# Kernel optimization log

Hardware: AMD Instinct MI355X
Metric: run time of the kernel (lower is better)

Reference implementation:

```python
import jax, jax.numpy as jnp
import numpy as np

PRUNING_RATE = 0.1
ROPE_THETA = 10000.0
EPS = 1e-5


def _rms_norm(x, w):
    v = jnp.mean(jnp.square(x.astype(jnp.float32)), axis=-1, keepdims=True)
    return (x * jax.lax.rsqrt(v + EPS)).astype(x.dtype) * w


def _rotate_half(x):
    x1, x2 = jnp.split(x, 2, axis=-1)
    return jnp.concatenate([-x2, x1], axis=-1)


def setup_inputs() -> dict:
    key = jax.random.key(0)
    ks = jax.random.split(key, 11)
    B, Q, D, H, Dh, P, F = 2, 16, 2048, 16, 128, 8192, 5632
    K = P + Q
    s = D ** -0.5
    inp = {
        "hidden_states": jax.random.normal(ks[0], (B, Q, D), jnp.float32),
        "past_k": jax.random.normal(ks[1], (B, H, P, Dh), jnp.float32),
        "past_v": jax.random.normal(ks[2], (B, H, P, Dh), jnp.float32),
        "wq": jax.random.normal(ks[3], (D, D), jnp.float32) * s,
        "wk": jax.random.normal(ks[4], (D, D), jnp.float32) * s,
        "wv": jax.random.normal(ks[5], (D, D), jnp.float32) * s,
        "wo": jax.random.normal(ks[6], (D, D), jnp.float32) * s,
        "w_gate": jax.random.normal(ks[7], (D, F), jnp.float32) * s,
        "w_up": jax.random.normal(ks[8], (D, F), jnp.float32) * s,
        "w_down": jax.random.normal(ks[9], (F, D), jnp.float32) * (F ** -0.5),
        "norm1_w": jnp.ones((D,), jnp.float32),
        "norm2_w": jnp.ones((D,), jnp.float32),
    }
    # causal mask over [past + new] keys: query i (global pos P+i) sees keys <= P+i
    q_pos = P + jnp.arange(Q)
    k_pos = jnp.arange(K)
    mask = jnp.where(k_pos[None, :] <= q_pos[:, None], 0.0, -1e9).astype(jnp.float32)
    inp["attn_mask"] = jnp.broadcast_to(mask[None, None], (B, 1, Q, K))
    return inp


def reference(hidden_states, past_k, past_v, attn_mask, wq, wk, wv, wo,
              w_gate, w_up, w_down, norm1_w, norm2_w):
    B, Q, D = hidden_states.shape
    _, H, P, Dh = past_k.shape
    K = P + Q

    residual = hidden_states
    x = _rms_norm(hidden_states, norm1_w)
    q = (x @ wq).reshape(B, Q, H, Dh).transpose(0, 2, 1, 3)  # [B,H,Q,Dh]
    k = (x @ wk).reshape(B, Q, H, Dh).transpose(0, 2, 1, 3)
    v = (x @ wv).reshape(B, Q, H, Dh).transpose(0, 2, 1, 3)

    # RoPE at cache positions P..P+Q-1 (past keys already rotated)
    inv_freq = 1.0 / (ROPE_THETA ** (jnp.arange(0, Dh, 2, dtype=jnp.float32) / Dh))
    pos = (P + jnp.arange(Q)).astype(jnp.float32)
    emb = jnp.concatenate([pos[:, None] * inv_freq[None, :]] * 2, axis=-1)  # [Q,Dh]
    cos, sin = jnp.cos(emb), jnp.sin(emb)
    q = q * cos + _rotate_half(q) * sin
    k = k * cos + _rotate_half(k) * sin

    k_full = jnp.concatenate([past_k, k], axis=2)  # [B,H,K,Dh]
    v_full = jnp.concatenate([past_v, v], axis=2)

    scores = jnp.einsum("bhqd,bhkd->bhqk", q, k_full) / jnp.sqrt(jnp.float32(Dh))
    scores = scores + attn_mask
    attn = jax.nn.softmax(scores, axis=-1)  # eager weights (output_attentions=True)
    out = jnp.einsum("bhqk,bhkd->bhqd", attn, v_full)
    out = out.transpose(0, 2, 1, 3).reshape(B, Q, D) @ wo
    h = residual + out

    y = _rms_norm(h, norm2_w)
    new_hidden = h + (jax.nn.silu(y @ w_gate) * (y @ w_up)) @ w_down

    # importance-based KV eviction: mean attn to last query over batch*heads
    imp = jnp.sum(attn[:, :, Q - 1, :], axis=(0, 1)) / (B * H)  # [K]
    imp = imp.at[K - 1].set(jnp.inf)  # never evict the last token's key
    n_prune = int(PRUNING_RATE * K)
    _, prune_idxs = jax.lax.top_k(-imp, n_prune)  # smallest-importance keys
    return new_hidden, attn, prune_idxs
```

## Files before the change

### kernel.cpp

```cpp
#include <hip/hip_runtime.h>
#include <math.h>

#define BB 2
#define QQ 16
#define DD 2048
#define HH 16
#define DHH 128
#define PP 8192
#define FF 5632
#define KK 8208
#define BH 32
#define RR 32
#define NPRUNE 820

#define OFF_X      0u
#define OFF_QR     65536u
#define OFF_KN     131072u
#define OFF_VN     196608u
#define OFF_ROWM   262144u
#define OFF_ROWZ   262656u
#define OFF_OATTN  263168u
#define OFF_H      328704u
#define OFF_Y      394240u
#define OFF_ACT    459776u
#define OFF_UNION  640064u
#define OFF_F64    (OFF_UNION + 4456448u)
#define D_X64      0u
#define D_K64      65536u
#define D_Q64      131072u
#define D_M64      135168u
#define D_Z64      135200u
#define D_SC       135232u
#define D_KEYS     397888u
#define OFF_RANK   (OFF_F64 + 812192u)

__global__ __launch_bounds__(256) void rmsnorm_kernel(
    const float* __restrict__ in, const float* __restrict__ w,
    float* __restrict__ out)
{
    int r = blockIdx.x;
    const float* x = in + (size_t)r * DD;
    float ss = 0.f;
    for (int c = threadIdx.x; c < DD; c += 256) { float v = x[c]; ss = fmaf(v, v, ss); }
    __shared__ float red[256];
    red[threadIdx.x] = ss;
    __syncthreads();
    for (int off = 128; off > 0; off >>= 1) {
        if (threadIdx.x < off) red[threadIdx.x] += red[threadIdx.x + off];
        __syncthreads();
    }
    float mean = red[0] / (float)DD;
    float scale = 1.0f / sqrtf(mean + 1e-5f);
    for (int c = threadIdx.x; c < DD; c += 256)
        out[(size_t)r * DD + c] = x[c] * scale * w[c];
}

__global__ __launch_bounds__(64) void rms32mix_kernel(
    const float* __restrict__ in, const float* __restrict__ w,
    double* __restrict__ out)
{
    int r = blockIdx.x;
    const float* x = in + (size_t)r * DD;
    __shared__ float bs[16];
    __shared__ float sscale;
    int tid = threadIdx.x;
    if (tid < 16) {
        const float* a = x + tid * 128;
        float rr[8];
#pragma unroll
        for (int j = 0; j < 8; ++j) { float v = a[j]; rr[j] = __fmul_rn(v, v); }
        for (int i = 8; i < 128; i += 8) {
#pragma unroll
            for (int j = 0; j < 8; ++j) {
                float v = a[i + j];
                rr[j] = __fadd_rn(rr[j], __fmul_rn(v, v));
            }
        }
        float t01 = __fadd_rn(rr[0], rr[1]);
        float t23 = __fadd_rn(rr[2], rr[3]);
        float t45 = __fadd_rn(rr[4], rr[5]);
        float t67 = __fadd_rn(rr[6], rr[7]);
        bs[tid] = __fadd_rn(__fadd_rn(t01, t23), __fadd_rn(t45, t67));
    }
    __syncthreads();
    if (tid == 0) {
        float c[8], d[4], e[2];
#pragma unroll
        for (int i = 0; i < 8; ++i) c[i] = __fadd_rn(bs[2 * i], bs[2 * i + 1]);
#pragma unroll
        for (int i = 0; i < 4; ++i) d[i] = __fadd_rn(c[2 * i], c[2 * i + 1]);
        e[0] = __fadd_rn(d[0], d[1]);
        e[1] = __fadd_rn(d[2], d[3]);
        float s = __fadd_rn(e[0], e[1]);
        float v = __fdiv_rn(s, 2048.0f);
        float ve = __fadd_rn(v, 1e-5f);
        float sq = __fsqrt_rn(ve);
        sscale = __fdiv_rn(1.0f, sq);
    }
    __syncthreads();
    double scd = (double)sscale;
    for (int c = tid; c < DD; c += 64)
        out[(size_t)r * DD + c] = ((double)x[c] * scd) * (double)w[c];
}

__global__ __launch_bounds__(256) void proj64_part_kernel(
    const double* __restrict__ x64, const float* __restrict__ wk,
    const float* __restrict__ wq, double* __restrict__ part)
{
    int cc = blockIdx.x, kc = blockIdx.y;
    int tid = threadIdx.x;
    int col = cc * 256 + tid;
    int d0 = kc * 64;
    __shared__ double xs[34 * 64];
    for (int i = tid; i < 34 * 64; i += 256) {
        int r = i >> 6, d = i & 63;
        int srcrow = (r < 32) ? r : ((r == 32) ? 15 : 31);
        xs[i] = x64[(size_t)srcrow * DD + d0 + d];
    }
    __syncthreads();
    double acc[34];
#pragma unroll
    for (int r = 0; r < 34; ++r) acc[r] = 0.0;
    const float* wkp = wk + (size_t)d0 * DD + col;
    const float* wqp = wq + (size_t)d0 * DD + col;
    for (int d = 0; d < 64; d += 4) {
        double wkb[4], wqb[4];
#pragma unroll
        for (int u = 0; u < 4; ++u) {
            wkb[u] = (double)wkp[(size_t)(d + u) * DD];
            wqb[u] = (double)wqp[(size_t)(d + u) * DD];
        }
#pragma unroll
        for (int u = 0; u < 4; ++u) {
#pragma unroll
            for (int r = 0; r < 32; ++r) acc[r] = fma(xs[r * 64 + d + u], wkb[u], acc[r]);
            acc[32] = fma(xs[32 * 64 + d + u], wqb[u], acc[32]);
            acc[33] = fma(xs[33 * 64 + d + u], wqb[u], acc[33]);
        }
    }
#pragma unroll
    for (int r = 0; r < 34; ++r)
        part[((size_t)kc * 34 + r) * DD + col] = acc[r];
}

__global__ __launch_bounds__(256) void proj64_reduce_kernel(
    const double* __restrict__ part, double* __restrict__ k64,
    double* __restrict__ q64)
{
    int e = blockIdx.x * 256 + threadIdx.x;
    if (e >= 34 * DD) return;
    int r = e >> 11, col = e & 2047;
    double s = 0.0;
#pragma unroll 8
    for (int kc = 0; kc < 32; ++kc) s += part[((size_t)kc * 34 + r) * DD + col];
    if (r < 32) k64[(size_t)r * DD + col] = s;
    else        q64[(size_t)(r - 32) * DD + col] = s;
}

__global__ __launch_bounds__(256) void rope64_kernel(
    double* __restrict__ k64, double* __restrict__ q64)
{
    int r = blockIdx.x;
    double* row;
    int pos;
    if (r < 32) { row = k64 + (size_t)r * DD; pos = PP + (r & 15); }
    else        { row = q64 + (size_t)(r - 32) * DD; pos = PP + 15; }
#pragma unroll 4
    for (int i = 0; i < 4; ++i) {
        int p = threadIdx.x + 256 * i;
        int h = p >> 6, j = p & 63;
        float pf = (float)pow(10000.0, (double)j / 64.0);
        float invf = __fdiv_rn(1.0f, pf);
        float ang = __fmul_rn((float)pos, invf);
        float cs = (float)cos((double)ang);
        float sn = (float)sin((double)ang);
        int c1 = h * DHH + j, c2 = c1 + 64;
        double v1 = row[c1], v2 = row[c2];
        row[c1] = v1 * (double)cs - v2 * (double)sn;
        row[c2] = v2 * (double)cs + v1 * (double)sn;
    }
}

template<int DCHUNK>
__global__ __launch_bounds__(256) void gemm32c2(
    const float* __restrict__ A, const float* __restrict__ w0,
    const float* __restrict__ w1, const float* __restrict__ w2,
    float* __restrict__ part, int Kdim, int N, size_t zstride)
{
    int cc = blockIdx.x, kc = blockIdx.y, z = blockIdx.z;
    int tid = threadIdx.x;
    int col0 = cc * 512 + tid;
    int d0 = kc * DCHUNK;
    const float* W = (z == 0) ? w0 : (z == 1) ? w1 : w2;
    __shared__ __align__(16) float xs[32 * DCHUNK];
    for (int i = tid; i < 32 * DCHUNK; i += 256) {
        int r = i / DCHUNK, d = i - r * DCHUNK;
        xs[i] = A[(size_t)r * Kdim + d0 + d];
    }
    __syncthreads();
    float acc0[32], acc1[32];
#pragma unroll
    for (int r = 0; r < 32; ++r) { acc0[r] = 0.f; acc1[r] = 0.f; }
// ... 9 lines not shown
        for (int r = 0; r < 32; ++r) {
            const float4 x0 = *(const float4*)(xs + r * DCHUNK + d);
            const float4 x1 = *(const float4*)(xs + r * DCHUNK + d + 4);
            float a = acc0[r], b = acc1[r];
            a = fmaf(x0.x, wb0[0], a);  b = fmaf(x0.x, wb1[0], b);
            a = fmaf(x0.y, wb0[1], a);  b = fmaf(x0.y, wb1[1], b);
            a = fmaf(x0.z, wb0[2], a);  b = fmaf(x0.z, wb1[2], b);
            a = fmaf(x0.w, wb0[3], a);  b = fmaf(x0.w, wb1[3], b);
            a = fmaf(x1.x, wb0[4], a);  b = fmaf(x1.x, wb1[4], b);
            a = fmaf(x1.y, wb0[5], a);  b = fmaf(x1.y, wb1[5], b);
            a = fmaf(x1.z, wb0[6], a);  b = fmaf(x1.z, wb1[6], b);
            a = fmaf(x1.w, wb0[7], a);  b = fmaf(x1.w, wb1[7], b);
            acc0[r] = a; acc1[r] = b;
        }
    }
    float* dst = part + (size_t)z * zstride;
#pragma unroll
    for (int r = 0; r < 32; ++r) {
        dst[((size_t)(kc * 32 + r)) * N + col0] = acc0[r];
        dst[((size_t)(kc * 32 + r)) * N + col0 + 256] = acc1[r];
    }
}

__global__ __launch_bounds__(256) void reduce_qkv_rope(
    const float* __restrict__ part, float* __restrict__ qr,
    float* __restrict__ kn, float* __restrict__ vn)
{
    int r = blockIdx.x;
    int b = r >> 4, qi = r & 15;
    int tid = threadIdx.x;
    int c = blockIdx.y * 256 + tid;
    int h = c >> 7, dh = c & 127, j = dh & 63;

    float invf = (float)exp(-((double)j / 64.0) * log(10000.0));
    float ang = (float)(PP + qi) * invf;
    float sn, cs;
    sincosf(ang, &sn, &cs);

    __shared__ float buf[256];
    size_t dsti = (((size_t)(b * HH + h)) * QQ + qi) * DHH + dh;
    for (int mat = 0; mat < 3; ++mat) {
        const float* pm = part + (size_t)mat * 64 * 65536 + (size_t)r * DD + c;
        float sa = 0.f, sb = 0.f;
#pragma unroll 8
        for (int kc = 0; kc < 32; ++kc) {
            sa += pm[(size_t)kc * 32 * DD];
            sb += pm[(size_t)(kc + 32) * 32 * DD];
        }
        float s = sa + sb;
        buf[tid] = s;
        __syncthreads();
        float val;
        if (mat == 2) {
            val = s;
        } else {
            float other = (dh < 64) ? -buf[tid + 64] : buf[tid - 64];
            val = s * cs + other * sn;
        }
        float* dst = (mat == 0) ? qr : (mat == 1) ? kn : vn;
        dst[dsti] = val;
        __syncthreads();
    }
}

__global__ __launch_bounds__(256) void scores_kernel(
    const float* __restrict__ qr, const float* __restrict__ past_k,
    const float* __restrict__ kn, float* __restrict__ attn,
    const double* __restrict__ q64, const double* __restrict__ k64,
    double* __restrict__ sc64)
{
    int bh = blockIdx.x, ch = blockIdx.y;
    int b = bh >> 4, h = bh & 15;
    int tid = threadIdx.x;
    __shared__ __align__(16) float qs[QQ * DHH];
    __shared__ double q64s[DHH];
    for (int i = tid; i < QQ * DHH; i += 256) qs[i] = qr[(size_t)bh * (QQ * DHH) + i];
    if (tid < DHH) q64s[tid] = q64[(size_t)b * DD + h * DHH + tid];
    __syncthreads();

    if (ch < 16) {
        int kbase = ch * 512;
        const float* kr0 = past_k + ((size_t)bh * PP + kbase + tid) * DHH;
        float acc[2][QQ];
#pragma unroll
// ... 60 lines not shown
#pragma unroll
            for (int q = 0; q < QQ; ++q) {
                float4 qv = *(const float4*)(qs + q * DHH + j * 4);
                acc[q] = fmaf(kv.x, qv.x, acc[q]);
                acc[q] = fmaf(kv.y, qv.y, acc[q]);
                acc[q] = fmaf(kv.z, qv.z, acc[q]);
                acc[q] = fmaf(kv.w, qv.w, acc[q]);
            }
        }
        int key = PP + tid;
#pragma unroll
        for (int q = 0; q < QQ; ++q) {
            float sv = acc[q] / 11.313708498984761f;
            if (key > PP + q) sv += -1e9f;
            attn[((size_t)(bh * QQ + q)) * KK + key] = sv;
        }
        double a64 = 0.0;
        const double* kd = k64 + (size_t)(b * QQ + tid) * DD + h * DHH;
        for (int j = 0; j < DHH; ++j) a64 = fma(kd[j], q64s[j], a64);
        sc64[(size_t)bh * KK + key] = a64 / (double)sqrtf(128.0f);
    }
}

__global__ __launch_bounds__(256) void rowstats_kernel(
    const float* __restrict__ attn, float* __restrict__ rowm, float* __restrict__ rowz)
{
    int row = blockIdx.x;
    const float* s = attn + (size_t)row * KK;
    float m = -INFINITY, z = 0.f;
    for (int k = threadIdx.x; k < KK; k += 256) {
        float v = s[k];
        float nm = fmaxf(m, v);
        z = z * expf(m - nm) + expf(v - nm);
        m = nm;
    }
    __shared__ float sm[256], sz[256];
    sm[threadIdx.x] = m; sz[threadIdx.x] = z;
    __syncthreads();
    for (int off = 128; off > 0; off >>= 1) {
        if (threadIdx.x < off) {
            float m1 = sm[threadIdx.x], z1 = sz[threadIdx.x];
            float m2 = sm[threadIdx.x + off], z2 = sz[threadIdx.x + off];
            float nm = fmaxf(m1, m2);
            sm[threadIdx.x] = nm;
            sz[threadIdx.x] = z1 * expf(m1 - nm) + z2 * expf(m2 - nm);
        }
        __syncthreads();
    }
    if (threadIdx.x == 0) { rowm[row] = sm[0]; rowz[row] = sz[0]; }
}

__global__ __launch_bounds__(256) void rowstats64_kernel(
    const double* __restrict__ sc, double* __restrict__ m64, double* __restrict__ z64)
{
    int row = blockIdx.x;
    const double* s = sc + (size_t)row * KK;
    double m = -INFINITY, z = 0.0;
    for (int k = threadIdx.x; k < KK; k += 256) {
        double v = s[k];
        double nm = fmax(m, v);
        z = z * exp(m - nm) + exp(v - nm);
        m = nm;
    }
    __shared__ double sm[256], sz[256];
    sm[threadIdx.x] = m; sz[threadIdx.x] = z;
    __syncthreads();
    for (int off = 128; off > 0; off >>= 1) {
        if (threadIdx.x < off) {
            double m1 = sm[threadIdx.x], z1 = sz[threadIdx.x];
            double m2 = sm[threadIdx.x + off], z2 = sz[threadIdx.x + off];
            double nm = fmax(m1, m2);
            sm[threadIdx.x] = nm;
            sz[threadIdx.x] = z1 * exp(m1 - nm) + z2 * exp(m2 - nm);
        }
        __syncthreads();
    }
    if (threadIdx.x == 0) { m64[row] = sm[0]; z64[row] = sz[0]; }
}

__global__ __launch_bounds__(256) void impkeys_kernel(
    const double* __restrict__ sc, const double* __restrict__ m64,
    const double* __restrict__ z64, unsigned long long* __restrict__ keys,
    int* __restrict__ rank)
{
    int k = blockIdx.x * 256 + threadIdx.x;
    if (k >= KK) return;
    rank[k] = 0;
    double t = 0.0;
    for (int bh = 0; bh < BH; ++bh)
        t += exp(sc[(size_t)bh * KK + k] - m64[bh]) / z64[bh];
    double imp = t / 32.0;
    if (k == KK - 1) imp = INFINITY;
    unsigned long long bits = (unsigned long long)__double_as_longlong(imp);
    keys[k] = (bits & ~0x3FFFull) | (unsigned long long)k;
}

__global__ __launch_bounds__(256) void rankpart_kernel(
    const unsigned long long* __restrict__ keys, int* __restrict__ rank)
{
    __shared__ unsigned long long chnk[1026];
    int gid = blockIdx.x * 256 + threadIdx.x;
    int base = blockIdx.y * 1026;
    for (int i = threadIdx.x; i < 1026; i += 256) chnk[i] = keys[base + i];
    __syncthreads();
    if (gid >= KK) return;
    unsigned long long mykey = keys[gid];
    int cnt = 0;
#pragma unroll 6
    for (int i = 0; i < 1026; ++i) cnt += (chnk[i] < mykey) ? 1 : 0;
    atomicAdd(&rank[gid], cnt);
}

__global__ __launch_bounds__(256) void rankwrite_kernel(
    const unsigned long long* __restrict__ keys, const int* __restrict__ rank,
    float* __restrict__ outp)
{
    int gid = blockIdx.x * 256 + threadIdx.x;
    if (gid >= KK) return;
    int r = rank[gid];
    if (r < NPRUNE)
        outp[r] = (float)(unsigned)(keys[gid] & 0x3FFFu);
}

__global__ __launch_bounds__(256) void pv_kernel(
    float* __restrict__ attn, const float* __restrict__ past_v,
    const float* __restrict__ vn, const float* __restrict__ rowm,
    const float* __restrict__ rowz, float* __restrict__ part)
{
    int bh = blockIdx.x, ch = blockIdx.y;
    int tid = threadIdx.x;
    __shared__ __align__(16) float p[QQ * 256];
    int nk = (ch < 32) ? 256 : 16;
    int kbase = ch * 256;
    if (tid < nk) {
        float sv[QQ];
#pragma unroll
        for (int q = 0; q < QQ; ++q)
            sv[q] = attn[((size_t)(bh * QQ + q)) * KK + kbase + tid];
#pragma unroll
        for (int q = 0; q < QQ; ++q) {
            int row = bh * QQ + q;
            float pv = expf(sv[q] - rowm[row]) / rowz[row];
            attn[((size_t)row) * KK + kbase + tid] = pv;
            p[q * 256 + tid] = pv;
        }
    }
    __syncthreads();

    int dq = tid & 31, q0 = tid >> 5;
    int d4 = dq * 4;
    float4 a0 = make_float4(0, 0, 0, 0), a1 = make_float4(0, 0, 0, 0);
    if (ch < 32) {
        const float* vbase = past_v + ((size_t)bh * PP + kbase) * DHH;
        for (int kk = 0; kk < 256; kk += 8) {
            float4 vb[8];
#pragma unroll
            for (int u = 0; u < 8; ++u)
                vb[u] = *(const float4*)(vbase + (size_t)(kk + u) * DHH + d4);
#pragma unroll
            for (int u = 0; u < 8; ++u) {
                float p0 = p[q0 * 256 + kk + u];
                float p1 = p[(q0 + 8) * 256 + kk + u];
                a0.x = fmaf(vb[u].x, p0, a0.x); a0.y = fmaf(vb[u].y, p0, a0.y);
                a0.z = fmaf(vb[u].z, p0, a0.z); a0.w = fmaf(vb[u].w, p0, a0.w);
                a1.x = fmaf(vb[u].x, p1, a1.x); a1.y = fmaf(vb[u].y, p1, a1.y);
                a1.z = fmaf(vb[u].z, p1, a1.z); a1.w = fmaf(vb[u].w, p1, a1.w);
            }
        }
    } else {
        const float* vbase = vn + (size_t)bh * QQ * DHH;
        for (int kk = 0; kk < 16; ++kk) {
            float4 v4 = *(const float4*)(vbase + (size_t)kk * DHH + d4);
            float p0 = p[q0 * 256 + kk];
            float p1 = p[(q0 + 8) * 256 + kk];
            a0.x = fmaf(v4.x, p0, a0.x); a0.y = fmaf(v4.y, p0, a0.y);
            a0.z = fmaf(v4.z, p0, a0.z); a0.w = fmaf(v4.w, p0, a0.w);
            a1.x = fmaf(v4.x, p1, a1.x); a1.y = fmaf(v4.y, p1, a1.y);
            a1.z = fmaf(v4.z, p1, a1.z); a1.w = fmaf(v4.w, p1, a1.w);
        }
    }
    size_t pb = ((size_t)ch * BH + bh) * (QQ * DHH);
    *(float4*)(part + pb + q0 * DHH + d4) = a0;
    *(float4*)(part + pb + (q0 + 8) * DHH + d4) = a1;
}

__global__ __launch_bounds__(256) void pv_reduce_kernel(
    const float* __restrict__ part, float* __restrict__ oattn)
{
    int e = blockIdx.x * 256 + threadIdx.x;
    float sa = 0.f, sb = 0.f;
#pragma unroll 8
    for (int ch = 0; ch < 16; ++ch) sa += part[(size_t)ch * 65536 + e];
#pragma unroll 8
    for (int ch = 16; ch < 33; ++ch) sb += part[(size_t)ch * 65536 + e];
    float s = sa + sb;
    int bh = e >> 11, rem = e & 2047, q = rem >> 7, d = rem & 127;
    int b = bh >> 4, h = bh & 15;
    oattn[((size_t)(b * QQ + q)) * DD + h * DHH + d] = s;
}

__global__ __launch_bounds__(256) void reduce_wo_kernel(
    const float* __restrict__ part, const float* __restrict__ resid,
    float* __restrict__ hbuf)
{
    int e = blockIdx.x * 256 + threadIdx.x;
    float sa = 0.f, sb = 0.f;
#pragma unroll 8
    for (int kc = 0; kc < 32; ++kc) {
        sa += part[(size_t)kc * 65536 + e];
        sb += part[(size_t)(kc + 32) * 65536 + e];
    }
    hbuf[e] = resid[e] + (sa + sb);
}

__global__ __launch_bounds__(256) void reduce_gateup_silu_kernel(
    const float* __restrict__ part, float* __restrict__ act)
{
    int e = blockIdx.x * 256 + threadIdx.x;
    float ga = 0.f, gb = 0.f, ua = 0.f, ub = 0.f;
#pragma unroll 8
    for (int kc = 0; kc < 16; ++kc) {
// ... 22 lines not shown
}

extern "C" void kernel_launch(void* const* d_in, const int* in_sizes, int n_in,
                              void* d_out, int out_size, void* d_ws, size_t ws_size,
                              hipStream_t stream)
{
    const float* hidden = (const float*)d_in[0];
    const float* past_k = (const float*)d_in[1];
    const float* past_v = (const float*)d_in[2];
    const float* wq     = (const float*)d_in[3];
    const float* wk     = (const float*)d_in[4];
    const float* wv     = (const float*)d_in[5];
    const float* wo     = (const float*)d_in[6];
    const float* wgate  = (const float*)d_in[7];
    const float* wup    = (const float*)d_in[8];
    const float* wdown  = (const float*)d_in[9];
    const float* n1w    = (const float*)d_in[10];
    const float* n2w    = (const float*)d_in[11];

    float* out_hidden = (float*)d_out;
    float* attn = out_hidden + (size_t)RR * DD;
    float* out_prune = attn + (size_t)BH * QQ * KK;
    float* ws = (float*)d_ws;
    double* f64 = (double*)(ws + OFF_F64);
    double* x64 = f64 + D_X64;
    double* k64 = f64 + D_K64;
    double* q64 = f64 + D_Q64;
    double* m64 = f64 + D_M64;
    double* z64 = f64 + D_Z64;
    double* sc64 = f64 + D_SC;
    unsigned long long* keys = (unsigned long long*)(f64 + D_KEYS);
    int* rank = (int*)(ws + OFF_RANK);
    double* part64 = (double*)(ws + OFF_UNION);

    rmsnorm_kernel<<<dim3(RR), dim3(256), 0, stream>>>(hidden, n1w, ws + OFF_X);

    gemm32c2<32><<<dim3(4, 64, 3), dim3(256), 0, stream>>>(
        ws + OFF_X, wq, wk, wv, ws + OFF_UNION, DD, DD, (size_t)64 * 65536);

    reduce_qkv_rope<<<dim3(RR, 8), dim3(256), 0, stream>>>(
        ws + OFF_UNION, ws + OFF_QR, ws + OFF_KN, ws + OFF_VN);

    rms32mix_kernel<<<dim3(RR), dim3(64), 0, stream>>>(hidden, n1w, x64);
    proj64_part_kernel<<<dim3(8, 32), dim3(256), 0, stream>>>(x64, wk, wq, part64);
    proj64_reduce_kernel<<<dim3(272), dim3(256), 0, stream>>>(part64, k64, q64);
    rope64_kernel<<<dim3(34), dim3(256), 0, stream>>>(k64, q64);

    scores_kernel<<<dim3(BH, 17), dim3(256), 0, stream>>>(
        ws + OFF_QR, past_k, ws + OFF_KN, attn, q64, k64, sc64);

    rowstats_kernel<<<dim3(BH * QQ), dim3(256), 0, stream>>>(
        attn, ws + OFF_ROWM, ws + OFF_ROWZ);
    rowstats64_kernel<<<dim3(BH), dim3(256), 0, stream>>>(sc64, m64, z64);
    impkeys_kernel<<<dim3(33), dim3(256), 0, stream>>>(sc64, m64, z64, keys, rank);
    rankpart_kernel<<<dim3(33, 8), dim3(256), 0, stream>>>(keys, rank);
    rankwrite_kernel<<<dim3(33), dim3(256), 0, stream>>>(keys, rank, out_prune);

    pv_kernel<<<dim3(BH, 33), dim3(256), 0, stream>>>(
        attn, past_v, ws + OFF_VN, ws + OFF_ROWM, ws + OFF_ROWZ, ws + OFF_UNION);

    pv_reduce_kernel<<<dim3(256), dim3(256), 0, stream>>>(ws + OFF_UNION, ws + OFF_OATTN);

    gemm32c2<32><<<dim3(4, 64, 1), dim3(256), 0, stream>>>(
        ws + OFF_OATTN, wo, wo, wo, ws + OFF_UNION, DD, DD, 0);

    reduce_wo_kernel<<<dim3(256), dim3(256), 0, stream>>>(ws + OFF_UNION, hidden, ws + OFF_H);

    rmsnorm_kernel<<<dim3(RR), dim3(256), 0, stream>>>(ws + OFF_H, n2w, ws + OFF_Y);

    gemm32c2<64><<<dim3(11, 32, 2), dim3(256), 0, stream>>>(
        ws + OFF_Y, wgate, wup, wup, ws + OFF_UNION, DD, FF, (size_t)32 * 180224);
    reduce_gateup_silu_kernel<<<dim3(704), dim3(256), 0, stream>>>(
        ws + OFF_UNION, ws + OFF_ACT);

    gemm32c2<32><<<dim3(4, 176, 1), dim3(256), 0, stream>>>(
        ws + OFF_ACT, wdown, wdown, wdown, ws + OFF_UNION, FF, DD, 0);
    reduce_down_kernel<<<dim3(256), dim3(256), 0, stream>>>(
        ws + OFF_UNION, ws + OFF_H, out_hidden);
}
```

Baseline: 379.8 us.

## Merge independent fp32 and fp64 side-path kernels into shared launches

Horizontally fuses independent kernels into single launches that dispatch on block index: the fp32 and fp64 RMS norms, the QKV GEMM with the fp64 K/Q projection, their reductions with RoPE folded in, the row-stats passes, PV with importance keys, PV reduce with rank partitioning, and the Wo GEMM with rank writing. The goal is to cut launch count and let the small, under-occupied fp64 pruning work run alongside the main fp32 path. A separate workspace region is added for the fp64 partials so they no longer alias the shared union buffer. The cost is larger register and shared-memory footprints per fused kernel, which can lower occupancy for the heavier branch.

Result: faster. 324.5 us (median of 2 runs) (-14.5%).

```diff
diff --git a/kernel.cpp b/kernel.cpp
--- a/kernel.cpp
+++ b/kernel.cpp
@@ -24,7 +24,8 @@
 #define OFF_Y      394240u
 #define OFF_ACT    459776u
 #define OFF_UNION  640064u
-#define OFF_F64    (OFF_UNION + 4456448u)
+#define OFF_P64P   (OFF_UNION + 12582912u)
+#define OFF_F64    (OFF_P64P + 4456448u)
 #define D_X64      0u
 #define D_K64      65536u
 #define D_Q64      131072u
@@ -55,129 +56,69 @@
         out[(size_t)r * DD + c] = x[c] * scale * w[c];
 }
 
-__global__ __launch_bounds__(64) void rms32mix_kernel(
+__global__ __launch_bounds__(256) void fused_rms_kernel(
     const float* __restrict__ in, const float* __restrict__ w,
-    double* __restrict__ out)
-{
-    int r = blockIdx.x;
-    const float* x = in + (size_t)r * DD;
+    float* __restrict__ out32, double* __restrict__ out64)
+{
+    int bx = blockIdx.x, tid = threadIdx.x;
+    __shared__ float red[256];
     __shared__ float bs[16];
     __shared__ float sscale;
-    int tid = threadIdx.x;
-    if (tid < 16) {
-        const float* a = x + tid * 128;
-        float rr[8];
-#pragma unroll
-        for (int j = 0; j < 8; ++j) { float v = a[j]; rr[j] = __fmul_rn(v, v); }
-        for (int i = 8; i < 128; i += 8) {
-#pragma unroll
-            for (int j = 0; j < 8; ++j) {
-                float v = a[i + j];
-                rr[j] = __fadd_rn(rr[j], __fmul_rn(v, v));
-            }
-        }
-        float t01 = __fadd_rn(rr[0], rr[1]);
-        float t23 = __fadd_rn(rr[2], rr[3]);
-        float t45 = __fadd_rn(rr[4], rr[5]);
-        float t67 = __fadd_rn(rr[6], rr[7]);
-        bs[tid] = __fadd_rn(__fadd_rn(t01, t23), __fadd_rn(t45, t67));
-    }
-    __syncthreads();
-    if (tid == 0) {
-        float c[8], d[4], e[2];
-#pragma unroll
-        for (int i = 0; i < 8; ++i) c[i] = __fadd_rn(bs[2 * i], bs[2 * i + 1]);
-#pragma unroll
-        for (int i = 0; i < 4; ++i) d[i] = __fadd_rn(c[2 * i], c[2 * i + 1]);
-        e[0] = __fadd_rn(d[0], d[1]);
-        e[1] = __fadd_rn(d[2], d[3]);
-        float s = __fadd_rn(e[0], e[1]);
-        float v = __fdiv_rn(s, 2048.0f);
-        float ve = __fadd_rn(v, 1e-5f);
-        float sq = __fsqrt_rn(ve);
-        sscale = __fdiv_rn(1.0f, sq);
-    }
-    __syncthreads();
-    double scd = (double)sscale;
-    for (int c = tid; c < DD; c += 64)
-        out[(size_t)r * DD + c] = ((double)x[c] * scd) * (double)w[c];
-}
-
-__global__ __launch_bounds__(256) void proj64_part_kernel(
-    const double* __restrict__ x64, const float* __restrict__ wk,
-    const float* __restrict__ wq, double* __restrict__ part)
-{
-    int cc = blockIdx.x, kc = blockIdx.y;
-    int tid = threadIdx.x;
-    int col = cc * 256 + tid;
-    int d0 = kc * 64;
-    __shared__ double xs[34 * 64];
-    for (int i = tid; i < 34 * 64; i += 256) {
-        int r = i >> 6, d = i & 63;
-        int srcrow = (r < 32) ? r : ((r == 32) ? 15 : 31);
-        xs[i] = x64[(size_t)srcrow * DD + d0 + d];
-    }
-    __syncthreads();
-    double acc[34];
-#pragma unroll
-    for (int r = 0; r < 34; ++r) acc[r] = 0.0;
-    const float* wkp = wk + (size_t)d0 * DD + col;
-    const float* wqp = wq + (size_t)d0 * DD + col;
-    for (int d = 0; d < 64; d += 4) {
-        double wkb[4], wqb[4];
-#pragma unroll
-        for (int u = 0; u < 4; ++u) {
-            wkb[u] = (double)wkp[(size_t)(d + u) * DD];
-            wqb[u] = (double)wqp[(size_t)(d + u) * DD];
-        }
-#pragma unroll
-        for (int u = 0; u < 4; ++u) {
-#pragma unroll
-            for (int r = 0; r < 32; ++r) acc[r] = fma(xs[r * 64 + d + u], wkb[u], acc[r]);
-            acc[32] = fma(xs[32 * 64 + d + u], wqb[u], acc[32]);
-            acc[33] = fma(xs[33 * 64 + d + u], wqb[u], acc[33]);
-        }
-    }
-#pragma unroll
-    for (int r = 0; r < 34; ++r)
-        part[((size_t)kc * 34 + r) * DD + col] = acc[r];
-}
-
-__global__ __launch_bounds__(256) void proj64_reduce_kernel(
-    const double* __restrict__ part, double* __restrict__ k64,
-    double* __restrict__ q64)
-{
-    int e = blockIdx.x * 256 + threadIdx.x;
-    if (e >= 34 * DD) return;
-    int r = e >> 11, col = e & 2047;
-    double s = 0.0;
-#pragma unroll 8
-    for (int kc = 0; kc < 32; ++kc) s += part[((size_t)kc * 34 + r) * DD + col];
-    if (r < 32) k64[(size_t)r * DD + col] = s;
-    else        q64[(size_t)(r - 32) * DD + col] = s;
-}
-
-__global__ __launch_bounds__(256) void rope64_kernel(
-    double* __restrict__ k64, double* __restrict__ q64)
-{
-    int r = blockIdx.x;
-    double* row;
-    int pos;
-    if (r < 32) { row = k64 + (size_t)r * DD; pos = PP + (r & 15); }
-    else        { row = q64 + (size_t)(r - 32) * DD; pos = PP + 15; }
-#pragma unroll 4
-    for (int i = 0; i < 4; ++i) {
-        int p = threadIdx.x + 256 * i;
-        int h = p >> 6, j = p & 63;
-        float pf = (float)pow(10000.0, (double)j / 64.0);
-        float invf = __fdiv_rn(1.0f, pf);
-        float ang = __fmul_rn((float)pos, invf);
-        float cs = (float)cos((double)ang);
-        float sn = (float)sin((double)ang);
-        int c1 = h * DHH + j, c2 = c1 + 64;
-        double v1 = row[c1], v2 = row[c2];
-        row[c1] = v1 * (double)cs - v2 * (double)sn;
-        row[c2] = v2 * (double)cs + v1 * (double)sn;
+    if (bx < 32) {
+        int r = bx;
+        const float* x = in + (size_t)r * DD;
+        float ss = 0.f;
+        for (int c = tid; c < DD; c += 256) { float v = x[c]; ss = fmaf(v, v, ss); }
+        red[tid] = ss;
+        __syncthreads();
+        for (int off = 128; off > 0; off >>= 1) {
+            if (tid < off) red[tid] += red[tid + off];
+            __syncthreads();
+        }
+        float mean = red[0] / (float)DD;
+        float scale = 1.0f / sqrtf(mean + 1e-5f);
+        for (int c = tid; c < DD; c += 256)
+            out32[(size_t)r * DD + c] = x[c] * scale * w[c];
+    } else {
+        int r = bx - 32;
+        const float* x = in + (size_t)r * DD;
+        if (tid < 16) {
+            const float* a = x + tid * 128;
+            float rr[8];
+#pragma unroll
+            for (int j = 0; j < 8; ++j) { float v = a[j]; rr[j] = __fmul_rn(v, v); }
+            for (int i = 8; i < 128; i += 8) {
+#pragma unroll
+                for (int j = 0; j < 8; ++j) {
+                    float v = a[i + j];
+                    rr[j] = __fadd_rn(rr[j], __fmul_rn(v, v));
+                }
+            }
+            float t01 = __fadd_rn(rr[0], rr[1]);
+            float t23 = __fadd_rn(rr[2], rr[3]);
+            float t45 = __fadd_rn(rr[4], rr[5]);
+            float t67 = __fadd_rn(rr[6], rr[7]);
+            bs[tid] = __fadd_rn(__fadd_rn(t01, t23), __fadd_rn(t45, t67));
+        }
+        __syncthreads();
+        if (tid == 0) {
+            float c[8], d[4], e[2];
+#pragma unroll
+            for (int i = 0; i < 8; ++i) c[i] = __fadd_rn(bs[2 * i], bs[2 * i + 1]);
+#pragma unroll
+            for (int i = 0; i < 4; ++i) d[i] = __fadd_rn(c[2 * i], c[2 * i + 1]);
+            e[0] = __fadd_rn(d[0], d[1]);
+            e[1] = __fadd_rn(d[2], d[3]);
+            float s = __fadd_rn(e[0], e[1]);
+            float v = __fdiv_rn(s, 2048.0f);
+            float ve = __fadd_rn(v, 1e-5f);
+            float sq = __fsqrt_rn(ve);
+            sscale = __fdiv_rn(1.0f, sq);
+        }
+        __syncthreads();
+        double scd = (double)sscale;
+        for (int c = tid; c < DD; c += 256)
+            out64[(size_t)r * DD + c] = ((double)x[c] * scd) * (double)w[c];
     }
 }
 
@@ -233,44 +174,156 @@
     }
 }
 
-__global__ __launch_bounds__(256) void reduce_qkv_rope(
+__global__ __launch_bounds__(256) void fused_qkv_p64_kernel(
+    const float* __restrict__ A, const float* __restrict__ wq,
+    const float* __restrict__ wk, const float* __restrict__ wv,
+    float* __restrict__ part, const double* __restrict__ x64,
+    double* __restrict__ p64)
+{
+    int bx = blockIdx.x, tid = threadIdx.x;
+    __shared__ __align__(16) float xs[32 * 32];
+    __shared__ double xs64[34 * 64];
+    if (bx < 768) {
+        int cc = bx & 3, kc = (bx >> 2) & 63, z = bx >> 8;
+        int col0 = cc * 512 + tid;
+        int d0 = kc * 32;
+        const float* W = (z == 0) ? wq : (z == 1) ? wk : wv;
+        for (int i = tid; i < 32 * 32; i += 256) {
+            int r = i >> 5, d = i & 31;
+            xs[i] = A[(size_t)r * DD + d0 + d];
+        }
+        __syncthreads();
+        float acc0[32], acc1[32];
+#pragma unroll
+        for (int r = 0; r < 32; ++r) { acc0[r] = 0.f; acc1[r] = 0.f; }
+        const float* wp = W + (size_t)d0 * DD + col0;
+        for (int d = 0; d < 32; d += 8) {
+            float wb0[8], wb1[8];
+#pragma unroll
+            for (int u = 0; u < 8; ++u) {
+                wb0[u] = wp[(size_t)(d + u) * DD];
+                wb1[u] = wp[(size_t)(d + u) * DD + 256];
+            }
+#pragma unroll
+            for (int r = 0; r < 32; ++r) {
+                const float4 x0 = *(const float4*)(xs + r * 32 + d);
+                const float4 x1 = *(const float4*)(xs + r * 32 + d + 4);
+                float a = acc0[r], b = acc1[r];
+                a = fmaf(x0.x, wb0[0], a);  b = fmaf(x0.x, wb1[0], b);
+                a = fmaf(x0.y, wb0[1], a);  b = fmaf(x0.y, wb1[1], b);
+                a = fmaf(x0.z, wb0[2], a);  b = fmaf(x0.z, wb1[2], b);
+                a = fmaf(x0.w, wb0[3], a);  b = fmaf(x0.w, wb1[3], b);
+                a = fmaf(x1.x, wb0[4], a);  b = fmaf(x1.x, wb1[4], b);
+                a = fmaf(x1.y, wb0[5], a);  b = fmaf(x1.y, wb1[5], b);
+                a = fmaf(x1.z, wb0[6], a);  b = fmaf(x1.z, wb1[6], b);
+                a = fmaf(x1.w, wb0[7], a);  b = fmaf(x1.w, wb1[7], b);
+                acc0[r] = a; acc1[r] = b;
+            }
+        }
+        float* dst = part + (size_t)z * 64 * 65536;
+#pragma unroll
+        for (int r = 0; r < 32; ++r) {
+            dst[((size_t)(kc * 32 + r)) * DD + col0] = acc0[r];
+            dst[((size_t)(kc * 32 + r)) * DD + col0 + 256] = acc1[r];
+        }
+    } else {
+        int p = bx - 768;
+        int cc = p & 7, kc = p >> 3;
+        int col = cc * 256 + tid;
+        int d0 = kc * 64;
+        for (int i = tid; i < 34 * 64; i += 256) {
+            int r = i >> 6, d = i & 63;
+            int srcrow = (r < 32) ? r : ((r == 32) ? 15 : 31);
+            xs64[i] = x64[(size_t)srcrow * DD + d0 + d];
+        }
+        __syncthreads();
+        double acc[34];
+#pragma unroll
+        for (int r = 0; r < 34; ++r) acc[r] = 0.0;
+        const float* wkp = wk + (size_t)d0 * DD + col;
+        const float* wqp = wq + (size_t)d0 * DD + col;
+        for (int d = 0; d < 64; d += 4) {
+            double wkb[4], wqb[4];
+#pragma unroll
+            for (int u = 0; u < 4; ++u) {
+                wkb[u] = (double)wkp[(size_t)(d + u) * DD];
+                wqb[u] = (double)wqp[(size_t)(d + u) * DD];
+            }
+#pragma unroll
+            for (int u = 0; u < 4; ++u) {
+#pragma unroll
+                for (int r = 0; r < 32; ++r) acc[r] = fma(xs64[r * 64 + d + u], wkb[u], acc[r]);
+                acc[32] = fma(xs64[32 * 64 + d + u], wqb[u], acc[32]);
+                acc[33] = fma(xs64[33 * 64 + d + u], wqb[u], acc[33]);
+            }
+        }
+#pragma unroll
+        for (int r = 0; r < 34; ++r)
+            p64[((size_t)kc * 34 + r) * DD + col] = acc[r];
+    }
+}
+
+__global__ __launch_bounds__(256) void fused_reduce_kernel(
     const float* __restrict__ part, float* __restrict__ qr,
-    float* __restrict__ kn, float* __restrict__ vn)
-{
-    int r = blockIdx.x;
-    int b = r >> 4, qi = r & 15;
-    int tid = threadIdx.x;
-    int c = blockIdx.y * 256 + tid;
-    int h = c >> 7, dh = c & 127, j = dh & 63;
-
-    float invf = (float)exp(-((double)j / 64.0) * log(10000.0));
-    float ang = (float)(PP + qi) * invf;
-    float sn, cs;
-    sincosf(ang, &sn, &cs);
-
+    float* __restrict__ kn, float* __restrict__ vn,
+    const double* __restrict__ p64, double* __restrict__ k64,
+    double* __restrict__ q64)
+{
+    int bx = blockIdx.x, tid = threadIdx.x;
     __shared__ float buf[256];
-    size_t dsti = (((size_t)(b * HH + h)) * QQ + qi) * DHH + dh;
-    for (int mat = 0; mat < 3; ++mat) {
-        const float* pm = part + (size_t)mat * 64 * 65536 + (size_t)r * DD + c;
-        float sa = 0.f, sb = 0.f;
+    __shared__ double dbuf[256];
+    if (bx < 256) {
+        int r = bx >> 3;
+        int b = r >> 4, qi = r & 15;
+        int c = (bx & 7) * 256 + tid;
+        int h = c >> 7, dh = c & 127, j = dh & 63;
+        float invf = (float)exp(-((double)j / 64.0) * log(10000.0));
+        float ang = (float)(PP + qi) * invf;
+        float sn, cs;
+        sincosf(ang, &sn, &cs);
+        size_t dsti = (((size_t)(b * HH + h)) * QQ + qi) * DHH + dh;
+        for (int mat = 0; mat < 3; ++mat) {
+            const float* pm = part + (size_t)mat * 64 * 65536 + (size_t)r * DD + c;
+            float sa = 0.f, sb = 0.f;
 #pragma unroll 8
-        for (int kc = 0; kc < 32; ++kc) {
-            sa += pm[(size_t)kc * 32 * DD];
-            sb += pm[(size_t)(kc + 32) * 32 * DD];
-        }
-        float s = sa + sb;
-        buf[tid] = s;
-        __syncthreads();
-        float val;
-        if (mat == 2) {
-            val = s;
-        } else {
-            float other = (dh < 64) ? -buf[tid + 64] : buf[tid - 64];
-            val = s * cs + other * sn;
-        }
-        float* dst = (mat == 0) ? qr : (mat == 1) ? kn : vn;
-        dst[dsti] = val;
-        __syncthreads();
+            for (int kc = 0; kc < 32; ++kc) {
+                sa += pm[(size_t)kc * 32 * DD];
+                sb += pm[(size_t)(kc + 32) * 32 * DD];
+            }
+            float s = sa + sb;
+            buf[tid] = s;
+            __syncthreads();
+            float val;
+            if (mat == 2) {
+                val = s;
+            } else {
+                float other = (dh < 64) ? -buf[tid + 64] : buf[tid - 64];
+                val = s * cs + other * sn;
+            }
+            float* dst = (mat == 0) ? qr : (mat == 1) ? kn : vn;
+            dst[dsti] = val;
+            __syncthreads();
+        }
+    } else {
+        int e = (bx - 256) * 256 + tid;
+        int r = e >> 11, col = e & 2047;
+        double s = 0.0;
+#pragma unroll 8
+        for (int kc = 0; kc < 32; ++kc) s += p64[((size_t)kc * 34 + r) * DD + col];
+        dbuf[tid] = s;
+        __syncthreads();
+        int dh = col & 127, j = dh & 63;
+        int pos = (r < 32) ? (PP + (r & 15)) : (PP + 15);
+        float pf = (float)pow(10000.0, (double)j / 64.0);
+        float invf = __fdiv_rn(1.0f, pf);
+        float ang = __fmul_rn((float)pos, invf);
+        float cs = (float)cos((double)ang);
+        float sn = (float)sin((double)ang);
+        double outv;
+        if (dh < 64) outv = s * (double)cs - dbuf[tid + 64] * (double)sn;
+        else         outv = s * (double)cs + dbuf[tid - 64] * (double)sn;
+        if (r < 32) k64[(size_t)r * DD + col] = outv;
+        else        q64[(size_t)(r - 32) * DD + col] = outv;
     }
 }
 
@@ -377,181 +430,229 @@
     }
 }
 
-__global__ __launch_bounds__(256) void rowstats_kernel(
-    const float* __restrict__ attn, float* __restrict__ rowm, float* __restrict__ rowz)
-{
-    int row = blockIdx.x;
-    const float* s = attn + (size_t)row * KK;
-    float m = -INFINITY, z = 0.f;
-    for (int k = threadIdx.x; k < KK; k += 256) {
-        float v = s[k];
-        float nm = fmaxf(m, v);
-        z = z * expf(m - nm) + expf(v - nm);
-        m = nm;
-    }
+__global__ __launch_bounds__(256) void fused_rowstats_kernel(
+    const float* __restrict__ attn, float* __restrict__ rowm, float* __restrict__ rowz,
+    const double* __restrict__ sc, double* __restrict__ m64, double* __restrict__ z64)
+{
+    int bx = blockIdx.x, tid = threadIdx.x;
     __shared__ float sm[256], sz[256];
-    sm[threadIdx.x] = m; sz[threadIdx.x] = z;
-    __syncthreads();
-    for (int off = 128; off > 0; off >>= 1) {
-        if (threadIdx.x < off) {
-            float m1 = sm[threadIdx.x], z1 = sz[threadIdx.x];
-            float m2 = sm[threadIdx.x + off], z2 = sz[threadIdx.x + off];
-            float nm = fmaxf(m1, m2);
-            sm[threadIdx.x] = nm;
-            sz[threadIdx.x] = z1 * expf(m1 - nm) + z2 * expf(m2 - nm);
-        }
-        __syncthreads();
-    }
-    if (threadIdx.x == 0) { rowm[row] = sm[0]; rowz[row] = sz[0]; }
-}
-
-__global__ __launch_bounds__(256) void rowstats64_kernel(
-    const double* __restrict__ sc, double* __restrict__ m64, double* __restrict__ z64)
-{
-    int row = blockIdx.x;
-    const double* s = sc + (size_t)row * KK;
-    double m = -INFINITY, z = 0.0;
-    for (int k = threadIdx.x; k < KK; k += 256) {
-        double v = s[k];
-        double nm = fmax(m, v);
-        z = z * exp(m - nm) + exp(v - nm);
-        m = nm;
-    }
-    __shared__ double sm[256], sz[256];
-    sm[threadIdx.x] = m; sz[threadIdx.x] = z;
-    __syncthreads();
-    for (int off = 128; off > 0; off >>= 1) {
-        if (threadIdx.x < off) {
-            double m1 = sm[threadIdx.x], z1 = sz[threadIdx.x];
-            double m2 = sm[threadIdx.x + off], z2 = sz[threadIdx.x + off];
-            double nm = fmax(m1, m2);
-            sm[threadIdx.x] = nm;
-            sz[threadIdx.x] = z1 * exp(m1 - nm) + z2 * exp(m2 - nm);
-        }
-        __syncthreads();
-    }
-    if (threadIdx.x == 0) { m64[row] = sm[0]; z64[row] = sz[0]; }
-}
-
-__global__ __launch_bounds__(256) void impkeys_kernel(
+    __shared__ double dm[256], dz[256];
+    if (bx < 512) {
+        int row = bx;
+        const float* s = attn + (size_t)row * KK;
+        float m = -INFINITY, z = 0.f;
+        for (int k = tid; k < KK; k += 256) {
+            float v = s[k];
+            float nm = fmaxf(m, v);
+            z = z * expf(m - nm) + expf(v - nm);
+            m = nm;
+        }
+        sm[tid] = m; sz[tid] = z;
+        __syncthreads();
+        for (int off = 128; off > 0; off >>= 1) {
+            if (tid < off) {
+                float m1 = sm[tid], z1 = sz[tid];
+                float m2 = sm[tid + off], z2 = sz[tid + off];
+                float nm = fmaxf(m1, m2);
+                sm[tid] = nm;
+                sz[tid] = z1 * expf(m1 - nm) + z2 * expf(m2 - nm);
+            }
+            __syncthreads();
+        }
+        if (tid == 0) { rowm[row] = sm[0]; rowz[row] = sz[0]; }
+    } else {
+        int row = bx - 512;
+        const double* s = sc + (size_t)row * KK;
+        double m = -INFINITY, z = 0.0;
+        for (int k = tid; k < KK; k += 256) {
+            double v = s[k];
+            double nm = fmax(m, v);
+            z = z * exp(m - nm) + exp(v - nm);
+            m = nm;
+        }
+        dm[tid] = m; dz[tid] = z;
+        __syncthreads();
+        for (int off = 128; off > 0; off >>= 1) {
+            if (tid < off) {
+                double m1 = dm[tid], z1 = dz[tid];
+                double m2 = dm[tid + off], z2 = dz[tid + off];
+                double nm = fmax(m1, m2);
+                dm[tid] = nm;
+                dz[tid] = z1 * exp(m1 - nm) + z2 * exp(m2 - nm);
+            }
+            __syncthreads();
+        }
+        if (tid == 0) { m64[row] = dm[0]; z64[row] = dz[0]; }
+    }
+}
+
+__global__ __launch_bounds__(256) void fused_pv_impkeys_kernel(
+    float* __restrict__ attn, const float* __restrict__ past_v,
+    const float* __restrict__ vn, const float* __restrict__ rowm,
+    const float* __restrict__ rowz, float* __restrict__ part,
     const double* __restrict__ sc, const double* __restrict__ m64,
     const double* __restrict__ z64, unsigned long long* __restrict__ keys,
     int* __restrict__ rank)
 {
-    int k = blockIdx.x * 256 + threadIdx.x;
-    if (k >= KK) return;
-    rank[k] = 0;
-    double t = 0.0;
-    for (int bh = 0; bh < BH; ++bh)
-        t += exp(sc[(size_t)bh * KK + k] - m64[bh]) / z64[bh];
-    double imp = t / 32.0;
-    if (k == KK - 1) imp = INFINITY;
-    unsigned long long bits = (unsigned long long)__double_as_longlong(imp);
-    keys[k] = (bits & ~0x3FFFull) | (unsigned long long)k;
-}
-
-__global__ __launch_bounds__(256) void rankpart_kernel(
+    int bx = blockIdx.x, tid = threadIdx.x;
+    __shared__ __align__(16) float p[QQ * 256];
+    if (bx < 1056) {
+        int bh = bx / 33, ch = bx - bh * 33;
+        int nk = (ch < 32) ? 256 : 16;
+        int kbase = ch * 256;
+        if (tid < nk) {
+            float sv[QQ];
+#pragma unroll
+            for (int q = 0; q < QQ; ++q)
+                sv[q] = attn[((size_t)(bh * QQ + q)) * KK + kbase + tid];
+#pragma unroll
+            for (int q = 0; q < QQ; ++q) {
+                int row = bh * QQ + q;
+                float pv = expf(sv[q] - rowm[row]) / rowz[row];
+                attn[((size_t)row) * KK + kbase + tid] = pv;
+                p[q * 256 + tid] = pv;
+            }
+        }
+        __syncthreads();
+
+        int dq = tid & 31, q0 = tid >> 5;
+        int d4 = dq * 4;
+        float4 a0 = make_float4(0, 0, 0, 0), a1 = make_float4(0, 0, 0, 0);
+        if (ch < 32) {
+            const float* vbase = past_v + ((size_t)bh * PP + kbase) * DHH;
+            for (int kk = 0; kk < 256; kk += 8) {
+                float4 vb[8];
+#pragma unroll
+                for (int u = 0; u < 8; ++u)
+                    vb[u] = *(const float4*)(vbase + (size_t)(kk + u) * DHH + d4);
+#pragma unroll
+                for (int u = 0; u < 8; ++u) {
+                    float p0 = p[q0 * 256 + kk + u];
+                    float p1 = p[(q0 + 8) * 256 + kk + u];
+                    a0.x = fmaf(vb[u].x, p0, a0.x); a0.y = fmaf(vb[u].y, p0, a0.y);
+                    a0.z = fmaf(vb[u].z, p0, a0.z); a0.w = fmaf(vb[u].w, p0, a0.w);
+                    a1.x = fmaf(vb[u].x, p1, a1.x); a1.y = fmaf(vb[u].y, p1, a1.y);
+                    a1.z = fmaf(vb[u].z, p1, a1.z); a1.w = fmaf(vb[u].w, p1, a1.w);
+                }
+            }
+        } else {
+            const float* vbase = vn + (size_t)bh * QQ * DHH;
+            for (int kk = 0; kk < 16; ++kk) {
+                float4 v4 = *(const float4*)(vbase + (size_t)kk * DHH + d4);
+                float p0 = p[q0 * 256 + kk];
+                float p1 = p[(q0 + 8) * 256 + kk];
+                a0.x = fmaf(v4.x, p0, a0.x); a0.y = fmaf(v4.y, p0, a0.y);
+                a0.z = fmaf(v4.z, p0, a0.z); a0.w = fmaf(v4.w, p0, a0.w);
+                a1.x = fmaf(v4.x, p1, a1.x); a1.y = fmaf(v4.y, p1, a1.y);
+                a1.z = fmaf(v4.z, p1, a1.z); a1.w = fmaf(v4.w, p1, a1.w);
+            }
+        }
+        size_t pb = ((size_t)ch * BH + bh) * (QQ * DHH);
+        *(float4*)(part + pb + q0 * DHH + d4) = a0;
+        *(float4*)(part + pb + (q0 + 8) * DHH + d4) = a1;
+    } else {
+        int k = (bx - 1056) * 256 + tid;
+        if (k >= KK) return;
+        rank[k] = 0;
+        double t = 0.0;
+        for (int bh = 0; bh < BH; ++bh)
+            t += exp(sc[(size_t)bh * KK + k] - m64[bh]) / z64[bh];
+        double imp = t / 32.0;
+        if (k == KK - 1) imp = INFINITY;
+        unsigned long long bits = (unsigned long long)__double_as_longlong(imp);
+        keys[k] = (bits & ~0x3FFFull) | (unsigned long long)k;
+    }
+}
+
+__global__ __launch_bounds__(256) void fused_pvred_rankpart_kernel(
+    const float* __restrict__ part, float* __restrict__ oattn,
     const unsigned long long* __restrict__ keys, int* __restrict__ rank)
 {
+    int bx = blockIdx.x, tid = threadIdx.x;
     __shared__ unsigned long long chnk[1026];
-    int gid = blockIdx.x * 256 + threadIdx.x;
-    int base = blockIdx.y * 1026;
-    for (int i = threadIdx.x; i < 1026; i += 256) chnk[i] = keys[base + i];
-    __syncthreads();
-    if (gid >= KK) return;
-    unsigned long long mykey = keys[gid];
-    int cnt = 0;
+    if (bx < 256) {
+        int e = bx * 256 + tid;
+        float sa = 0.f, sb = 0.f;
+#pragma unroll 8
+        for (int ch = 0; ch < 16; ++ch) sa += part[(size_t)ch * 65536 + e];
+#pragma unroll 8
+        for (int ch = 16; ch < 33; ++ch) sb += part[(size_t)ch * 65536 + e];
+        float s = sa + sb;
+        int bh = e >> 11, rem = e & 2047, q = rem >> 7, d = rem & 127;
+        int b = bh >> 4, h = bh & 15;
+        oattn[((size_t)(b * QQ + q)) * DD + h * DHH + d] = s;
+    } else {
+        int idx = bx - 256;
+        int xb = idx % 33, yb = idx / 33;
+        int gid = xb * 256 + tid;
+        int base = yb * 1026;
+        for (int i = tid; i < 1026; i += 256) chnk[i] = keys[base + i];
+        __syncthreads();
+        if (gid >= KK) return;
+        unsigned long long mykey = keys[gid];
+        int cnt = 0;
 #pragma unroll 6
-    for (int i = 0; i < 1026; ++i) cnt += (chnk[i] < mykey) ? 1 : 0;
-    atomicAdd(&rank[gid], cnt);
-}
-
-__global__ __launch_bounds__(256) void rankwrite_kernel(
+        for (int i = 0; i < 1026; ++i) cnt += (chnk[i] < mykey) ? 1 : 0;
+        atomicAdd(&rank[gid], cnt);
+    }
+}
+
+__global__ __launch_bounds__(256) void fused_wogemm_rankwrite_kernel(
+    const float* __restrict__ A, const float* __restrict__ wo,
+    float* __restrict__ part,
     const unsigned long long* __restrict__ keys, const int* __restrict__ rank,
     float* __restrict__ outp)
 {
-    int gid = blockIdx.x * 256 + threadIdx.x;
-    if (gid >= KK) return;
-    int r = rank[gid];
-    if (r < NPRUNE)
-        outp[r] = (float)(unsigned)(keys[gid] & 0x3FFFu);
-}
-
-__global__ __launch_bounds__(256) void pv_kernel(
-    float* __restrict__ attn, const float* __restrict__ past_v,
-    const float* __restrict__ vn, const float* __restrict__ rowm,
-    const float* __restrict__ rowz, float* __restrict__ part)
-{
-    int bh = blockIdx.x, ch = blockIdx.y;
-    int tid = threadIdx.x;
-    __shared__ __align__(16) float p[QQ * 256];
-    int nk = (ch < 32) ? 256 : 16;
-    int kbase = ch * 256;
-    if (tid < nk) {
-        float sv[QQ];
-#pragma unroll
-        for (int q = 0; q < QQ; ++q)
-            sv[q] = attn[((size_t)(bh * QQ + q)) * KK + kbase + tid];
-#pragma unroll
-        for (int q = 0; q < QQ; ++q) {
-            int row = bh * QQ + q;
-            float pv = expf(sv[q] - rowm[row]) / rowz[row];
-            attn[((size_t)row) * KK + kbase + tid] = pv;
-            p[q * 256 + tid] = pv;
-        }
-    }
-    __syncthreads();
-
-    int dq = tid & 31, q0 = tid >> 5;
-    int d4 = dq * 4;
-    float4 a0 = make_float4(0, 0, 0, 0), a1 = make_float4(0, 0, 0, 0);
-    if (ch < 32) {
-        const float* vbase = past_v + ((size_t)bh * PP + kbase) * DHH;
-        for (int kk = 0; kk < 256; kk += 8) {
-            float4 vb[8];
-#pragma unroll
-            for (int u = 0; u < 8; ++u)
-                vb[u] = *(const float4*)(vbase + (size_t)(kk + u) * DHH + d4);
+    int bx = blockIdx.x, tid = threadIdx.x;
+    __shared__ __align__(16) float xs[32 * 32];
+    if (bx < 256) {
+        int cc = bx & 3, kc = bx >> 2;
+        int col0 = cc * 512 + tid;
+        int d0 = kc * 32;
+        for (int i = tid; i < 32 * 32; i += 256) {
+            int r = i >> 5, d = i & 31;
+            xs[i] = A[(size_t)r * DD + d0 + d];
+        }
+        __syncthreads();
+        float acc0[32], acc1[32];
+#pragma unroll
+        for (int r = 0; r < 32; ++r) { acc0[r] = 0.f; acc1[r] = 0.f; }
+        const float* wp = wo + (size_t)d0 * DD + col0;
+        for (int d = 0; d < 32; d += 8) {
+            float wb0[8], wb1[8];
 #pragma unroll
             for (int u = 0; u < 8; ++u) {
-                float p0 = p[q0 * 256 + kk + u];
-                float p1 = p[(q0 + 8) * 256 + kk + u];
-                a0.x = fmaf(vb[u].x, p0, a0.x); a0.y = fmaf(vb[u].y, p0, a0.y);
-                a0.z = fmaf(vb[u].z, p0, a0.z); a0.w = fmaf(vb[u].w, p0, a0.w);
-                a1.x = fmaf(vb[u].x, p1, a1.x); a1.y = fmaf(vb[u].y, p1, a1.y);
-                a1.z = fmaf(vb[u].z, p1, a1.z); a1.w = fmaf(vb[u].w, p1, a1.w);
-            }
+                wb0[u] = wp[(size_t)(d + u) * DD];
+                wb1[u] = wp[(size_t)(d + u) * DD + 256];
+            }
+#pragma unroll
+            for (int r = 0; r < 32; ++r) {
+                const float4 x0 = *(const float4*)(xs + r * 32 + d);
+                const float4 x1 = *(const float4*)(xs + r * 32 + d + 4);
+                float a = acc0[r], b = acc1[r];
+                a = fmaf(x0.x, wb0[0], a);  b = fmaf(x0.x, wb1[0], b);
+                a = fmaf(x0.y, wb0[1], a);  b = fmaf(x0.y, wb1[1], b);
+                a = fmaf(x0.z, wb0[2], a);  b = fmaf(x0.z, wb1[2], b);
+                a = fmaf(x0.w, wb0[3], a);  b = fmaf(x0.w, wb1[3], b);
+                a = fmaf(x1.x, wb0[4], a);  b = fmaf(x1.x, wb1[4], b);
+                a = fmaf(x1.y, wb0[5], a);  b = fmaf(x1.y, wb1[5], b);
+                a = fmaf(x1.z, wb0[6], a);  b = fmaf(x1.z, wb1[6], b);
+                a = fmaf(x1.w, wb0[7], a);  b = fmaf(x1.w, wb1[7], b);
+                acc0[r] = a; acc1[r] = b;
+            }
+        }
+#pragma unroll
+        for (int r = 0; r < 32; ++r) {
+            part[((size_t)(kc * 32 + r)) * DD + col0] = acc0[r];
+            part[((size_t)(kc * 32 + r)) * DD + col0 + 256] = acc1[r];
         }
     } else {
-        const float* vbase = vn + (size_t)bh * QQ * DHH;
-        for (int kk = 0; kk < 16; ++kk) {
-            float4 v4 = *(const float4*)(vbase + (size_t)kk * DHH + d4);
-            float p0 = p[q0 * 256 + kk];
-            float p1 = p[(q0 + 8) * 256 + kk];
-            a0.x = fmaf(v4.x, p0, a0.x); a0.y = fmaf(v4.y, p0, a0.y);
-            a0.z = fmaf(v4.z, p0, a0.z); a0.w = fmaf(v4.w, p0, a0.w);
-            a1.x = fmaf(v4.x, p1, a1.x); a1.y = fmaf(v4.y, p1, a1.y);
-            a1.z = fmaf(v4.z, p1, a1.z); a1.w = fmaf(v4.w, p1, a1.w);
-        }
-    }
-    size_t pb = ((size_t)ch * BH + bh) * (QQ * DHH);
-    *(float4*)(part + pb + q0 * DHH + d4) = a0;
-    *(float4*)(part + pb + (q0 + 8) * DHH + d4) = a1;
-}
-
-__global__ __launch_bounds__(256) void pv_reduce_kernel(
-    const float* __restrict__ part, float* __restrict__ oattn)
-{
-    int e = blockIdx.x * 256 + threadIdx.x;
-    float sa = 0.f, sb = 0.f;
-#pragma unroll 8
-    for (int ch = 0; ch < 16; ++ch) sa += part[(size_t)ch * 65536 + e];
-#pragma unroll 8
-    for (int ch = 16; ch < 33; ++ch) sb += part[(size_t)ch * 65536 + e];
-    float s = sa + sb;
-    int bh = e >> 11, rem = e & 2047, q = rem >> 7, d = rem & 127;
-    int b = bh >> 4, h = bh & 15;
-    oattn[((size_t)(b * QQ + q)) * DD + h * DHH + d] = s;
+        int gid = (bx - 256) * 256 + tid;
+        if (gid >= KK) return;
+        int r = rank[gid];
+        if (r < NPRUNE)
+            outp[r] = (float)(unsigned)(keys[gid] & 0x3FFFu);
+    }
 }
 
 __global__ __launch_bounds__(256) void reduce_wo_kernel(
@@ -620,6 +721,7 @@
     float* attn = out_hidden + (size_t)RR * DD;
     float* out_prune = attn + (size_t)BH * QQ * KK;
     float* ws = (float*)d_ws;
+    double* p64part = (double*)(ws + OFF_P64P);
     double* f64 = (double*)(ws + OFF_F64);
     double* x64 = f64 + D_X64;
     double* k64 = f64 + D_K64;
@@ -629,38 +731,30 @@
     double* sc64 = f64 + D_SC;
     unsigned long long* keys = (unsigned long long*)(f64 + D_KEYS);
     int* rank = (int*)(ws + OFF_RANK);
-    double* part64 = (double*)(ws + OFF_UNION);
-
-    rmsnorm_kernel<<<dim3(RR), dim3(256), 0, stream>>>(hidden, n1w, ws + OFF_X);
-
-    gemm32c2<32><<<dim3(4, 64, 3), dim3(256), 0, stream>>>(
-        ws + OFF_X, wq, wk, wv, ws + OFF_UNION, DD, DD, (size_t)64 * 65536);
-
-    reduce_qkv_rope<<<dim3(RR, 8), dim3(256), 0, stream>>>(
-        ws + OFF_UNION, ws + OFF_QR, ws + OFF_KN, ws + OFF_VN);
-
-    rms32mix_kernel<<<dim3(RR), dim3(64), 0, stream>>>(hidden, n1w, x64);
-    proj64_part_kernel<<<dim3(8, 32), dim3(256), 0, stream>>>(x64, wk, wq, part64);
-    proj64_reduce_kernel<<<dim3(272), dim3(256), 0, stream>>>(part64, k64, q64);
-    rope64_kernel<<<dim3(34), dim3(256), 0, stream>>>(k64, q64);
+
+    fused_rms_kernel<<<dim3(64), dim3(256), 0, stream>>>(hidden, n1w, ws + OFF_X, x64);
+
+    fused_qkv_p64_kernel<<<dim3(1024), dim3(256), 0, stream>>>(
+        ws + OFF_X, wq, wk, wv, ws + OFF_UNION, x64, p64part);
+
+    fused_reduce_kernel<<<dim3(528), dim3(256), 0, stream>>>(
+        ws + OFF_UNION, ws + OFF_QR, ws + OFF_KN, ws + OFF_VN, p64part, k64, q64);
 
     scores_kernel<<<dim3(BH, 17), dim3(256), 0, stream>>>(
         ws + OFF_QR, past_k, ws + OFF_KN, attn, q64, k64, sc64);
 
-    rowstats_kernel<<<dim3(BH * QQ), dim3(256), 0, stream>>>(
-        attn, ws + OFF_ROWM, ws + OFF_ROWZ);
-    rowstats64_kernel<<<dim3(BH), dim3(256), 0, stream>>>(sc64, m64, z64);
-    impkeys_kernel<<<dim3(33), dim3(256), 0, stream>>>(sc64, m64, z64, keys, rank);
-    rankpart_kernel<<<dim3(33, 8), dim3(256), 0, stream>>>(keys, rank);
-    rankwrite_kernel<<<dim3(33), dim3(256), 0, stream>>>(keys, rank, out_prune);
-
-    pv_kernel<<<dim3(BH, 33), dim3(256), 0, stream>>>(
-        attn, past_v, ws + OFF_VN, ws + OFF_ROWM, ws + OFF_ROWZ, ws + OFF_UNION);
-
-    pv_reduce_kernel<<<dim3(256), dim3(256), 0, stream>>>(ws + OFF_UNION, ws + OFF_OATTN);
-
-    gemm32c2<32><<<dim3(4, 64, 1), dim3(256), 0, stream>>>(
-        ws + OFF_OATTN, wo, wo, wo, ws + OFF_UNION, DD, DD, 0);
+    fused_rowstats_kernel<<<dim3(544), dim3(256), 0, stream>>>(
+        attn, ws + OFF_ROWM, ws + OFF_ROWZ, sc64, m64, z64);
+
+    fused_pv_impkeys_kernel<<<dim3(1089), dim3(256), 0, stream>>>(
+        attn, past_v, ws + OFF_VN, ws + OFF_ROWM, ws + OFF_ROWZ, ws + OFF_UNION,
+        sc64, m64, z64, keys, rank);
+
+    fused_pvred_rankpart_kernel<<<dim3(520), dim3(256), 0, stream>>>(
+        ws + OFF_UNION, ws + OFF_OATTN, keys, rank);
+
+    fused_wogemm_rankwrite_kernel<<<dim3(289), dim3(256), 0, stream>>>(
+        ws + OFF_OATTN, wo, ws + OFF_UNION, keys, rank, out_prune);
 
     reduce_wo_kernel<<<dim3(256), dim3(256), 0, stream>>>(ws + OFF_UNION, hidden, ws + OFF_H);
 
```
